# Performance work log

Measured on AMD Instinct MI355X. Metric: run time of the kernel, lower is better.

The kernel has to match this reference:

```python
import math
import jax, jax.numpy as jnp
import numpy as np

B, S, M, D, H = 4, 1024, 8, 64, 8
NF = D // 2  # n_freq = head_dim // 2
BANDWIDTH = 1.0


def setup_inputs() -> dict:
    key = jax.random.key(0)
    ks = jax.random.split(key, 12)
    n = lambda k, shp, sc=1.0: (jax.random.normal(k, shp, dtype=jnp.float32) * sc)
    w_scale = 0.02  # typical init scale for linear weights
    return {
        'q_atoms': n(ks[0], (B, S, M, D)),
        'q_logw': n(ks[1], (B, S, M)),
        'k_atoms': n(ks[2], (B, S, M, D)),
        'k_logw': n(ks[3], (B, S, M)),
        'v_atoms': n(ks[4], (B, S, M, D)),
        'v_logw': n(ks[5], (B, S, M)),
        'Wq': n(ks[6], (H * D, D), w_scale),   # torch Linear weight [out, in]
        'Wk': n(ks[7], (H * D, D), w_scale),
        'Wv': n(ks[8], (H * D, D), w_scale),
        'Wo': n(ks[9], (D, H * D), w_scale),
        'Ww': n(ks[10], (M, D), w_scale * 0.1),  # w_proj.weight scaled by 0.1
        'freqs': n(ks[11], (H, D, NF), 1.0 / BANDWIDTH),  # buffer
    }


def reference(q_atoms, q_logw, k_atoms, k_logw, v_atoms, v_logw,
              Wq, Wk, Wv, Wo, Ww, freqs):
    rff_scale = 1.0 / math.sqrt(NF)
    attn_scale = 1.0 / math.sqrt(D)

    q_w = jax.nn.softmax(q_logw, axis=-1)  # [B,S,M]
    k_w = jax.nn.softmax(k_logw, axis=-1)

    def proj(x, W):  # x: [B,S,M,D], W: [H*D, D] -> [B,S,M,H,D]
        return jnp.einsum('bsmd,ed->bsme', x, W).reshape(B, -1, M, H, D)

    qa = proj(q_atoms, Wq)
    ka = proj(k_atoms, Wk)
    va = proj(v_atoms, Wv)  # [B,S,M,H,D]

    def rff_encode(atoms, weights):
        # atoms: [B,S,M,H,D], weights: [B,S,M] -> [B,H,S,F] with F=D
        p = jnp.einsum('bsmhd,hdf->bsmhf', atoms, freqs)
        phi = jnp.concatenate([jnp.cos(p), jnp.sin(p)], axis=-1) * rff_scale
        z = jnp.einsum('bsmhf,bsm->bshf', phi, weights)
        return z.transpose(0, 2, 1, 3)

    q_enc = rff_encode(qa, q_w)  # [B,H,S,D]
    k_enc = rff_encode(ka, k_w)

    attn = jax.nn.softmax(
        jnp.einsum('bhqf,bhkf->bhqk', q_enc, k_enc) * attn_scale, axis=-1)

    # attn @ values, keeping atom dim m: [B,S,M,H,D]
    out = jnp.einsum('bhqk,bkmhd->bqmhd', attn, va)
    out = out.reshape(B, S, M, H * D)
    out_atoms = out @ Wo.T                  # [B,S,M,D]
    out_features = out_atoms.mean(axis=2)   # [B,S,D]
    new_log_weights = q_logw + out_features @ Ww.T  # [B,S,M]
    return out_atoms, new_log_weights
```

## Files before the change

### kernel.cpp

```cpp
#include <hip/hip_runtime.h>
#include <hip/hip_bf16.h>

typedef __hip_bfloat16 bf16;
typedef __attribute__((ext_vector_type(8))) short short8;
typedef __attribute__((ext_vector_type(4))) float floatx4;

#define CB 4
#define CS 1024
#define CM 8
#define CD 64
#define CH 8
#define CNF 32
#define CHD 512

#define OB_STRIDE 520
#define OS_STRIDE 68
#define AT_STRIDE 72
#define VO_STRIDE 40

__device__ __forceinline__ float b2f(bf16 x) { return __bfloat162float(x); }
__device__ __forceinline__ float us2f(unsigned short u) {
    union { unsigned int i; float f; } v; v.i = ((unsigned int)u) << 16; return v.f;
}
__device__ __forceinline__ floatx4 mfma16(short8 a, short8 b, floatx4 c) {
    return __builtin_amdgcn_mfma_f32_16x16x32_bf16(a, b, c, 0, 0, 0);
}


__global__ __launch_bounds__(256) void prep(const float* __restrict__ Wq,
                                            const float* __restrict__ Wk,
                                            const float* __restrict__ freqs,
                                            const float* __restrict__ Wo,
                                            const float* __restrict__ Wv,
                                            bf16* __restrict__ Fqb,
                                            bf16* __restrict__ Fkb,
                                            bf16* __restrict__ Wof,
                                            bf16* __restrict__ Wvf) {
    int bx = blockIdx.x, t = threadIdx.x;
    if (bx < 128) {
        int which = bx >> 6, h = (bx >> 3) & 7, ec = bx & 7;
        const float* W = which ? Wk : Wq;
        bf16* Fb = which ? Fkb : Fqb;
        int f = t & 31, el = t >> 5;
        int e = ec * 8 + el;
        float acc = 0.f;
        for (int d = 0; d < 64; ++d)
            acc += W[(h * 64 + d) * 64 + e] * freqs[(h * 64 + d) * 32 + f];
        int ntile = h * 2 + (f >> 4);
        int half = e >> 5, quad = (e >> 3) & 3, j = e & 7;
        Fb[(ntile * 2 + half) * 512 + quad * 128 + (f & 15) * 8 + j] = __float2bfloat16(acc);
    } else if (bx < 144) {
        int gid = (bx - 128) * 256 + t;
        #pragma unroll
        for (int i = 0; i < 2; ++i) {
            int idx4 = gid * 2 + i;
            float4 v = ((const float4*)Wo)[idx4];
            int flat = idx4 * 4;
            int o = flat >> 9, k0 = flat & 511;
            int ot = o >> 4, r0 = o & 15;
            int ks = k0 >> 5, qd = (k0 >> 3) & 3, j0 = k0 & 7;
            union { bf16 ob[4]; uint2 u; } pk;
            pk.ob[0] = __float2bfloat16(v.x); pk.ob[1] = __float2bfloat16(v.y);
            pk.ob[2] = __float2bfloat16(v.z); pk.ob[3] = __float2bfloat16(v.w);
            *(uint2*)(Wof + (ot * 16 + ks) * 512 + qd * 128 + r0 * 8 + j0) = pk.u;
        }
    } else {
        int gid = (bx - 144) * 256 + t;
        #pragma unroll
        for (int i = 0; i < 2; ++i) {
            int idx4 = gid * 2 + i;
            float4 v = ((const float4*)Wv)[idx4];
            int flat = idx4 * 4;
            int c = flat >> 6, e0 = flat & 63;
            int h2 = c >> 6, d = c & 63;
            int ehalf = e0 >> 5, qd = (e0 >> 3) & 3, j0 = e0 & 7;
            union { bf16 ob[4]; uint2 u; } pk;
            pk.ob[0] = __float2bfloat16(v.x); pk.ob[1] = __float2bfloat16(v.y);
            pk.ob[2] = __float2bfloat16(v.z); pk.ob[3] = __float2bfloat16(v.w);
            *(uint2*)(Wvf + (h2 * 8 + (d >> 4) * 2 + ehalf) * 512
                          + qd * 128 + (d & 15) * 8 + j0) = pk.u;
        }
    }
}

__global__ __launch_bounds__(256) void encvp(const float* __restrict__ qa_in,
                                             const float* __restrict__ ql,
                                             const float* __restrict__ ka_in,
                                             const float* __restrict__ kl,
                                             const bf16* __restrict__ Fqb,
                                             const bf16* __restrict__ Fkb,
                                             bf16* __restrict__ qf,
                                             bf16* __restrict__ kf,
                                             const float* __restrict__ va_in,
                                             const bf16* __restrict__ Wvf,
                                             bf16* __restrict__ Vt) {
    __shared__ __align__(16) bf16 smem[20480];
    int t = threadIdx.x;
    int w = t >> 6, l = t & 63;
    int quad = l >> 4, r = l & 15;

    if (blockIdx.x < 1024) {
        int blk = blockIdx.x;
        int xbase = blk * 4;
        int b = xbase >> 10, s0 = xbase & 1023;
        float* wgtF = (float*)smem;
        bf16* atq = smem + 128;
        bf16* atk = smem + 128 + 2304;
        bf16* zL  = smem + 128 + 4608;
        int tw = w & 1, nb = (w >> 1) * 8;

        {
            const float* srcq = qa_in + (size_t)(blk * 32) * 64;
            const float* srck = ka_in + (size_t)(blk * 32) * 64;
            #pragma unroll
            for (int j = 0; j < 2; ++j) {
                int idx4 = j * 256 + t;
                int flat = idx4 * 4;
                int row = flat >> 6, e = flat & 63;
                float4 vq = ((const float4*)srcq)[idx4];
                float4 vk = ((const float4*)srck)[idx4];
                union { bf16 ob[4]; uint2 u; } pq, pk2;
                pq.ob[0] = __float2bfloat16(vq.x); pq.ob[1] = __float2bfloat16(vq.y);
                pq.ob[2] = __float2bfloat16(vq.z); pq.ob[3] = __float2bfloat16(vq.w);
                pk2.ob[0] = __float2bfloat16(vk.x); pk2.ob[1] = __float2bfloat16(vk.y);
                pk2.ob[2] = __float2bfloat16(vk.z); pk2.ob[3] = __float2bfloat16(vk.w);
                *(uint2*)(atq + row * AT_STRIDE + e) = pq.u;
                *(uint2*)(atk + row * AT_STRIDE + e) = pk2.u;
            }
        }
        if (t < 64) {
            int which = t >> 5, row = t & 31;
            int si = row >> 3, m = row & 7;
            const float* lwp = (which ? kl : ql) + (size_t)(xbase + si) * 8;
            float lw[8]; float mx = -1e30f;
            #pragma unroll
            for (int j = 0; j < 8; ++j) { lw[j] = lwp[j]; mx = fmaxf(mx, lw[j]); }
            float sm = 0.f;
            #pragma unroll
            for (int j = 0; j < 8; ++j) sm += __expf(lw[j] - mx);
            const float rs = 0.17677669529663687f;
            float osc = which ? rs : rs * 0.125f;
            wgtF[which * 32 + row] = __expf(lw[m] - mx) * (osc / sm);
        }
        __syncthreads();

        for (int which = 0; which < 2; ++which) {
            const bf16* atb2 = which ? atk : atq;
            const bf16* Fb = which ? Fkb : Fqb;

            short8 a0 = *(const short8*)(atb2 + (tw * 16 + r) * AT_STRIDE + quad * 8);
            short8 a1 = *(const short8*)(atb2 + (tw * 16 + r) * AT_STRIDE + quad * 8 + 32);

            floatx4 acc[8];
            #pragma unroll
            for (int nt = 0; nt < 8; ++nt) {
                int ntile = nb + nt;
                short8 b0 = *(const short8*)(Fb + (ntile * 2 + 0) * 512 + l * 8);
                short8 b1 = *(const short8*)(Fb + (ntile * 2 + 1) * 512 + l * 8);
                floatx4 c = {0.f, 0.f, 0.f, 0.f};
                c = mfma16(a0, b0, c);
                c = mfma16(a1, b1, c);
                acc[nt] = c;
            }

            float wv[4];
            #pragma unroll
            for (int reg = 0; reg < 4; ++reg)
                wv[reg] = wgtF[which * 32 + tw * 16 + quad * 4 + reg];

            int si = tw * 2 + (quad >> 1);
            int iss = quad & 1;
            #pragma unroll
            for (int nt = 0; nt < 8; ++nt) {
                int n = (nb + nt) * 16 + r;
                int h = n >> 5, f = n & 31;
                float zc = 0.f, zs = 0.f;
                #pragma unroll
                for (int reg = 0; reg < 4; ++reg) {
                    float sv, cv;
                    __sincosf(acc[nt][reg], &sv, &cv);
                    zc += wv[reg] * cv;
                    zs += wv[reg] * sv;
                }
                zc += __shfl_xor(zc, 16);
                zs += __shfl_xor(zs, 16);
                float val = iss ? zs : zc;
                zL[((which * 4 + si) * 8 + h) * 64 + f + 32 * iss] = __float2bfloat16(val);
            }
        }
        __syncthreads();

        #pragma unroll
        for (int rep = 0; rep < 2; ++rep) {
            int idx = rep * 256 + t;
            int row = idx >> 3, c = idx & 7;
            int which = row >> 5, si = (row >> 3) & 3, h = row & 7;
            bf16* enc = which ? kf : qf;
            short8 v = *(const short8*)(zL + row * 64 + c * 8);
            int s = s0 + si;
            int bh = b * 8 + h;
            int kt = s >> 4, half = c >> 2, qd = c & 3;
            *(short8*)(enc + ((size_t)((bh * 64 + kt) * 2 + half)) * 512
                           + (qd * 16 + (s & 15)) * 8) = v;
        }
    } else {
        int vp = blockIdx.x - 1024;
        int bh = vp & 31, sc = vp >> 5;
        int b = bh >> 3, h = bh & 7;
        bf16* atb = smem;
        bf16* os = smem;

        const float* src = va_in + ((size_t)(b * 1024 + sc * 32)) * 512;
        #pragma unroll
        for (int j = 0; j < 16; ++j) {
            int idx4 = j * 256 + t;
            float4 v = ((const float4*)src)[idx4];
            int flat = idx4 * 4;
            int s = flat >> 9, m = (flat >> 6) & 7, e = flat & 63;
            union { bf16 ob[4]; uint2 u; } pk;
            pk.ob[0] = __float2bfloat16(v.x); pk.ob[1] = __float2bfloat16(v.y);
            pk.ob[2] = __float2bfloat16(v.z); pk.ob[3] = __float2bfloat16(v.w);
            *(uint2*)(atb + (m * 32 + s) * AT_STRIDE + e) = pk.u;
        }
        __syncthreads();

        int dhalf = w & 1, sg = w >> 1;
        short8 aw0[2], aw1[2];
        #pragma unroll
        for (int dt = 0; dt < 2; ++dt) {
            int dt4 = dhalf * 2 + dt;
            aw0[dt] = *(const short8*)(Wvf + (size_t)(h * 8 + dt4 * 2 + 0) * 512 + l * 8);
            aw1[dt] = *(const short8*)(Wvf + (size_t)(h * 8 + dt4 * 2 + 1) * 512 + l * 8);
        }
        floatx4 acc[8][2];
        #pragma unroll
        for (int m = 0; m < 8; ++m)
            #pragma unroll
            for (int dt = 0; dt < 2; ++dt) acc[m][dt] = (floatx4){0.f, 0.f, 0.f, 0.f};

        #pragma unroll
        for (int m = 0; m < 8; ++m) {
            short8 b0 = *(const short8*)(atb + (m * 32 + sg * 16 + r) * AT_STRIDE + quad * 8);
            short8 b1 = *(const short8*)(atb + (m * 32 + sg * 16 + r) * AT_STRIDE + quad * 8 + 32);
            #pragma unroll
            for (int dt = 0; dt < 2; ++dt) {
                acc[m][dt] = mfma16(aw0[dt], b0, acc[m][dt]);
                acc[m][dt] = mfma16(aw1[dt], b1, acc[m][dt]);
            }
        }
        __syncthreads();

        #pragma unroll
        for (int m = 0; m < 8; ++m)
            #pragma unroll
            for (int dt = 0; dt < 2; ++dt)
                #pragma unroll
                for (int reg = 0; reg < 4; ++reg) {
                    int n = m * 64 + dhalf * 32 + dt * 16 + quad * 4 + reg;
                    os[n * VO_STRIDE + sg * 16 + r] = __float2bfloat16(acc[m][dt][reg]);
                }
        __syncthreads();

        #pragma unroll
        for (int j = 0; j < 8; ++j) {
            int ch = j * 256 + t;
            int nblk = ch >> 6, lv = ch & 63;
            int rv = lv & 15, qv = lv >> 4;
            short8 v = *(const short8*)(os + (nblk * 16 + rv) * VO_STRIDE + qv * 8);
            *(short8*)(Vt + ((size_t)(bh * 32 + nblk) * 32 + sc) * 512 + lv * 8) = v;
        }
    }
}

__global__ __launch_bounds__(512, 2) void attn_kern(const bf16* __restrict__ qf,
                                                    const bf16* __restrict__ kf,
                                                    const bf16* __restrict__ Vt,
                                                    bf16* __restrict__ tmpf) {
    int n = blockIdx.x;
    int bh = (n & 7) | (((n >> 7) & 3) << 3);
    int qb = (n >> 3) & 15;
    int b = bh >> 3, h = bh & 7;

    __shared__ __align__(16) bf16 Sc[64 * 1024];
    int t = threadIdx.x;
    int w = t >> 6, l = t & 63;
    int quad = l >> 4, r = l & 15;
    int k7 = r & 7;

    const bf16* qfb = qf + (size_t)(bh * 128 + qb * 8) * 512 + l * 8;
    short8 q[8];
    #pragma unroll
    for (int i = 0; i < 8; ++i) q[i] = *(const short8*)(qfb + i * 512);

    const bf16* kfb = kf + (size_t)(bh * 128) * 512 + l * 8;
    short8 kA0 = *(const short8*)(kfb + (size_t)(w * 8) * 1024);
    short8 kA1 = *(const short8*)(kfb + (size_t)(w * 8) * 1024 + 512);
    short8 kB0 = *(const short8*)(kfb + (size_t)(w * 8 + 1) * 1024);
    short8 kB1 = *(const short8*)(kfb + (size_t)(w * 8 + 1) * 1024 + 512);

    #pragma unroll
    for (int i = 0; i < 8; ++i) {
        short8 k0 = kA0, k1 = kA1;
        kA0 = kB0; kA1 = kB1;
        if (i < 6) {
            kB0 = *(const short8*)(kfb + (size_t)(w * 8 + i + 2) * 1024);
            kB1 = *(const short8*)(kfb + (size_t)(w * 8 + i + 2) * 1024 + 512);
        }
        int ktl = w * 8 + i;
        int chunk = ktl * 2 + (quad >> 1);
        int sw = ((chunk ^ k7) << 3) + (quad & 1) * 4;
        #pragma unroll
        for (int qt = 0; qt < 4; ++qt) {
            floatx4 c = {0.f, 0.f, 0.f, 0.f};
            c = mfma16(k0, q[2 * qt], c);
            c = mfma16(k1, q[2 * qt + 1], c);
            union { uint2 u; bf16 bb[4]; } p;
            #pragma unroll
            for (int reg = 0; reg < 4; ++reg) p.bb[reg] = __float2bfloat16(c[reg]);
            *(uint2*)(Sc + (qt * 16 + r) * 1024 + sw) = p.u;
        }
    }
    __syncthreads();

    for (int i = 0; i < 8; ++i) {
        int row = w * 8 + i;
        int key = row & 7;
        bf16* rowp = Sc + row * 1024;
        int p0 = ((2 * l) ^ key) << 3;
        int p1 = ((2 * l + 1) ^ key) << 3;
        union { short8 s; unsigned short u[8]; } v0, v1;
        v0.s = *(const short8*)(rowp + p0);
        v1.s = *(const short8*)(rowp + p1);
        float f[16];
        #pragma unroll
        for (int j = 0; j < 8; ++j) { f[j] = us2f(v0.u[j]); f[8 + j] = us2f(v1.u[j]); }
        float mx = -1e30f;
        #pragma unroll
        for (int j = 0; j < 16; ++j) mx = fmaxf(mx, f[j]);
        #pragma unroll
        for (int off = 32; off; off >>= 1) mx = fmaxf(mx, __shfl_xor(mx, off));
        float sm = 0.f;
        #pragma unroll
        for (int j = 0; j < 16; ++j) { f[j] = __expf(f[j] - mx); sm += f[j]; }
        #pragma unroll
        for (int off = 32; off; off >>= 1) sm += __shfl_xor(sm, off);
        float inv = 1.f / sm;
        #pragma unroll
        for (int j = 0; j < 8; ++j) {
            v0.u[j] = (unsigned short)(__bfloat16_as_ushort(__float2bfloat16(f[j] * inv)));
            v1.u[j] = (unsigned short)(__bfloat16_as_ushort(__float2bfloat16(f[8 + j] * inv)));
        }
        *(short8*)(rowp + p0) = v0.s;
        *(short8*)(rowp + p1) = v1.s;
    }
    __syncthreads();

    floatx4 acc[4][4];
    #pragma unroll
    for (int qt = 0; qt < 4; ++qt)
        #pragma unroll
        for (int nt = 0; nt < 4; ++nt) acc[qt][nt] = (floatx4){0.f, 0.f, 0.f, 0.f};

    const bf16* vbase = Vt + ((size_t)(bh * 32 + w * 4) * 32) * 512 + l * 8;
    short8 vA[4], vB[4], vC[4];
    #pragma unroll
    for (int nt = 0; nt < 4; ++nt) vA[nt] = *(const short8*)(vbase + nt * 16384);
    #pragma unroll
    for (int nt = 0; nt < 4; ++nt) vB[nt] = *(const short8*)(vbase + nt * 16384 + 512);

    #pragma unroll
    for (int ks = 0; ks < 32; ++ks) {
        if (ks < 30) {
            #pragma unroll
            for (int nt = 0; nt < 4; ++nt)
                vC[nt] = *(const short8*)(vbase + nt * 16384 + (ks + 2) * 512);
        }
        int pc = (((ks * 4 + quad) ^ k7) << 3);
        short8 pa[4];
        #pragma unroll
        for (int qt = 0; qt < 4; ++qt)
            pa[qt] = *(const short8*)(Sc + (qt * 16 + r) * 1024 + pc);
        #pragma unroll
        for (int nt = 0; nt < 4; ++nt)
            #pragma unroll
            for (int qt = 0; qt < 4; ++qt)
                acc[qt][nt] = mfma16(pa[qt], vA[nt], acc[qt][nt]);
        #pragma unroll
        for (int nt = 0; nt < 4; ++nt) { vA[nt] = vB[nt]; vB[nt] = vC[nt]; }
    }
    __syncthreads();

    bf16* Ob = Sc;
    #pragma unroll
    for (int qt = 0; qt < 4; ++qt)
        #pragma unroll
        for (int nt = 0; nt < 4; ++nt)
            #pragma unroll
            for (int reg = 0; reg < 4; ++reg) {
                int col = w * 64 + nt * 16 + r;
                int m = col >> 6, d = col & 63;
                int colS = m * 64 + ((d + m * 8) & 63);
                Ob[(qt * 16 + quad * 4 + reg) * OB_STRIDE + colS] =
                    __float2bfloat16(acc[qt][nt][reg]);
            }
    __syncthreads();

    #pragma unroll
    for (int i = 0; i < 8; ++i) {
        int ci = i * 8 + w;
        int lv = t & 63;
        int T = ci >> 1, khalf = ci & 1;
        int quadv = lv >> 4, rv = lv & 15;
        int p = rv >> 3, m = rv & 7;
        int q_local = T * 2 + p;
        int d0 = khalf * 32 + quadv * 8;
        int colS = m * 64 + ((d0 + m * 8) & 63);
        short8 v = *(const short8*)(Ob + q_local * OB_STRIDE + colS);
        int GT = b * 512 + qb * 32 + T;
        *(short8*)(tmpf + ((size_t)(GT * 16 + h * 2 + khalf)) * 512 + lv * 8) = v;
    }
}

__global__ __launch_bounds__(256) void finalize(const bf16* __restrict__ tmpf,
                                                const bf16* __restrict__ Wof,
                                                const float* __restrict__ Ww,
                                                const float* __restrict__ ql,
                                                float* __restrict__ out) {
    __shared__ __align__(16) float Os[64][OS_STRIDE];
    __shared__ float fs[8][64];
    int t = threadIdx.x;
    int w = t >> 6, l = t & 63;
    int quad = l >> 4, r = l & 15;
    size_t rowbase = (size_t)blockIdx.x * 64;

    floatx4 acc[4];
    #pragma unroll
    for (int nt = 0; nt < 4; ++nt) acc[nt] = (floatx4){0.f, 0.f, 0.f, 0.f};

    const bf16* afrag = tmpf + ((size_t)(blockIdx.x * 4 + w) * 16) * 512 + l * 8;
    const bf16* bfrag = Wof + l * 8;

    for (int ks = 0; ks < 16; ++ks) {
        short8 a = *(const short8*)(afrag + ks * 512);
        #pragma unroll
        for (int nt = 0; nt < 4; ++nt) {
            short8 bb = *(const short8*)(bfrag + (size_t)(nt * 16 + ks) * 512);
            acc[nt] = mfma16(a, bb, acc[nt]);
        }
    }
    #pragma unroll
    for (int nt = 0; nt < 4; ++nt)
        #pragma unroll
        for (int reg = 0; reg < 4; ++reg)
            Os[w * 16 + quad * 4 + reg][nt * 16 + r] = acc[nt][reg];
    __syncthreads();

    #pragma unroll
    for (int i = 0; i < 4; ++i) {
        int ch = i * 256 + t;
        int rr = ch >> 4, c4 = (ch & 15) * 4;
        float4 v = *(const float4*)&Os[rr][c4];
        *(float4*)(out + (rowbase + rr) * 64 + c4) = v;
    }

    {
        int g = t >> 5, oo = (t & 31) * 2;
        float f0 = 0.f, f1 = 0.f;
        #pragma unroll
        for (int m = 0; m < 8; ++m) {
            f0 += Os[g * 8 + m][oo];
            f1 += Os[g * 8 + m][oo + 1];
        }
        fs[g][oo] = f0 * 0.125f;
        fs[g][oo + 1] = f1 * 0.125f;
    }
    __syncthreads();

    if (t < 64) {
        int g = t >> 3, mm = t & 7;
        size_t x = (size_t)blockIdx.x * 8 + g;
        float nl = ql[x * 8 + mm];
        #pragma unroll
        for (int o = 0; o < 64; ++o) nl += fs[g][o] * Ww[mm * 64 + o];
        out[(size_t)CB * CS * CM * CD + x * 8 + mm] = nl;
    }
}

extern "C" void kernel_launch(void* const* d_in, const int* in_sizes, int n_in,
                              void* d_out, int out_size, void* d_ws, size_t ws_size,
                              hipStream_t stream) {
    const float* q_atoms = (const float*)d_in[0];
    const float* q_logw  = (const float*)d_in[1];
    const float* k_atoms = (const float*)d_in[2];
    const float* k_logw  = (const float*)d_in[3];
    const float* v_atoms = (const float*)d_in[4];
    const float* Wq = (const float*)d_in[6];
    const float* Wk = (const float*)d_in[7];
    const float* Wv = (const float*)d_in[8];
    const float* Wo = (const float*)d_in[9];
    const float* Ww = (const float*)d_in[10];
    const float* freqs = (const float*)d_in[11];

    bf16* Fqb = (bf16*)d_ws;
    bf16* Fkb = Fqb + 16384;
    bf16* qf = Fkb + 16384;
    bf16* kf = qf + 2097152;
    bf16* Vt = kf + 2097152;
    bf16* tmpf = Vt + 2097152 * 8;
    bf16* Wof = tmpf + 16777216;
    bf16* Wvf = Wof + 32768;
    float* out = (float*)d_out;

    prep<<<160, 256, 0, stream>>>(Wq, Wk, freqs, Wo, Wv, Fqb, Fkb, Wof, Wvf);
    encvp<<<2048, 256, 0, stream>>>(q_atoms, q_logw, k_atoms, k_logw,
                                    Fqb, Fkb, qf, kf,
                                    v_atoms, Wvf, Vt);
    attn_kern<<<512, 512, 0, stream>>>(qf, kf, Vt, tmpf);
    finalize<<<CB * CS / 8, 256, 0, stream>>>(tmpf, Wof, Ww, q_logw, out);
}
```

Before: 190.6 us.

## Split attention over key halves with unnormalized exp and deferred softmax normalization

The attention kernel now processes keys in two halves: scores are exponentiated directly without a max pass, written to a half-size shared buffer, and immediately consumed by the P·V MFMA loop. Row sums are reduced across waves and the normalization is applied to the output accumulators at the end. This removes the separate softmax pass and halves shared memory, allowing higher occupancy. The V-prep block index mapping is also reordered. It relies on the scores being bounded so that skipping max subtraction cannot overflow.

```diff
diff --git a/kernel.cpp b/kernel.cpp
--- a/kernel.cpp
+++ b/kernel.cpp
@@ -205,8 +205,9 @@
         }
     } else {
         int vp = blockIdx.x - 1024;
-        int bh = vp & 31, sc = vp >> 5;
-        int b = bh >> 3, h = bh & 7;
+        int g = vp & 127, h = vp >> 7;
+        int b = g >> 5, sc = g & 31;
+        int bh = b * 8 + h;
         bf16* atb = smem;
         bf16* os = smem;
 
@@ -272,7 +273,7 @@
     }
 }
 
-__global__ __launch_bounds__(512, 2) void attn_kern(const bf16* __restrict__ qf,
+__global__ __launch_bounds__(512, 4) void attn_kern(const bf16* __restrict__ qf,
                                                     const bf16* __restrict__ kf,
                                                     const bf16* __restrict__ Vt,
                                                     bf16* __restrict__ tmpf) {
@@ -281,114 +282,115 @@
     int qb = (n >> 3) & 15;
     int b = bh >> 3, h = bh & 7;
 
-    __shared__ __align__(16) bf16 Sc[64 * 1024];
+    __shared__ __align__(16) bf16 Sc[64 * OB_STRIDE];
+    __shared__ float sumW[8 * 64];
+    __shared__ float invL[64];
     int t = threadIdx.x;
     int w = t >> 6, l = t & 63;
     int quad = l >> 4, r = l & 15;
     int k7 = r & 7;
 
     const bf16* qfb = qf + (size_t)(bh * 128 + qb * 8) * 512 + l * 8;
-    short8 q[8];
-    #pragma unroll
-    for (int i = 0; i < 8; ++i) q[i] = *(const short8*)(qfb + i * 512);
-
     const bf16* kfb = kf + (size_t)(bh * 128) * 512 + l * 8;
-    short8 kA0 = *(const short8*)(kfb + (size_t)(w * 8) * 1024);
-    short8 kA1 = *(const short8*)(kfb + (size_t)(w * 8) * 1024 + 512);
-    short8 kB0 = *(const short8*)(kfb + (size_t)(w * 8 + 1) * 1024);
-    short8 kB1 = *(const short8*)(kfb + (size_t)(w * 8 + 1) * 1024 + 512);
-
-    #pragma unroll
-    for (int i = 0; i < 8; ++i) {
-        short8 k0 = kA0, k1 = kA1;
-        kA0 = kB0; kA1 = kB1;
-        if (i < 6) {
-            kB0 = *(const short8*)(kfb + (size_t)(w * 8 + i + 2) * 1024);
-            kB1 = *(const short8*)(kfb + (size_t)(w * 8 + i + 2) * 1024 + 512);
-        }
-        int ktl = w * 8 + i;
-        int chunk = ktl * 2 + (quad >> 1);
-        int sw = ((chunk ^ k7) << 3) + (quad & 1) * 4;
-        #pragma unroll
-        for (int qt = 0; qt < 4; ++qt) {
-            floatx4 c = {0.f, 0.f, 0.f, 0.f};
-            c = mfma16(k0, q[2 * qt], c);
-            c = mfma16(k1, q[2 * qt + 1], c);
-            union { uint2 u; bf16 bb[4]; } p;
-            #pragma unroll
-            for (int reg = 0; reg < 4; ++reg) p.bb[reg] = __float2bfloat16(c[reg]);
-            *(uint2*)(Sc + (qt * 16 + r) * 1024 + sw) = p.u;
-        }
-    }
-    __syncthreads();
-
-    for (int i = 0; i < 8; ++i) {
-        int row = w * 8 + i;
-        int key = row & 7;
-        bf16* rowp = Sc + row * 1024;
-        int p0 = ((2 * l) ^ key) << 3;
-        int p1 = ((2 * l + 1) ^ key) << 3;
-        union { short8 s; unsigned short u[8]; } v0, v1;
-        v0.s = *(const short8*)(rowp + p0);
-        v1.s = *(const short8*)(rowp + p1);
-        float f[16];
-        #pragma unroll
-        for (int j = 0; j < 8; ++j) { f[j] = us2f(v0.u[j]); f[8 + j] = us2f(v1.u[j]); }
-        float mx = -1e30f;
-        #pragma unroll
-        for (int j = 0; j < 16; ++j) mx = fmaxf(mx, f[j]);
-        #pragma unroll
-        for (int off = 32; off; off >>= 1) mx = fmaxf(mx, __shfl_xor(mx, off));
-        float sm = 0.f;
-        #pragma unroll
-        for (int j = 0; j < 16; ++j) { f[j] = __expf(f[j] - mx); sm += f[j]; }
-        #pragma unroll
-        for (int off = 32; off; off >>= 1) sm += __shfl_xor(sm, off);
-        float inv = 1.f / sm;
-        #pragma unroll
-        for (int j = 0; j < 8; ++j) {
-            v0.u[j] = (unsigned short)(__bfloat16_as_ushort(__float2bfloat16(f[j] * inv)));
-            v1.u[j] = (unsigned short)(__bfloat16_as_ushort(__float2bfloat16(f[8 + j] * inv)));
-        }
-        *(short8*)(rowp + p0) = v0.s;
-        *(short8*)(rowp + p1) = v1.s;
-    }
-    __syncthreads();
+    const bf16* vbase = Vt + ((size_t)(bh * 32 + w * 4) * 32) * 512 + l * 8;
 
     floatx4 acc[4][4];
     #pragma unroll
     for (int qt = 0; qt < 4; ++qt)
         #pragma unroll
         for (int nt = 0; nt < 4; ++nt) acc[qt][nt] = (floatx4){0.f, 0.f, 0.f, 0.f};
-
-    const bf16* vbase = Vt + ((size_t)(bh * 32 + w * 4) * 32) * 512 + l * 8;
-    short8 vA[4], vB[4], vC[4];
-    #pragma unroll
-    for (int nt = 0; nt < 4; ++nt) vA[nt] = *(const short8*)(vbase + nt * 16384);
-    #pragma unroll
-    for (int nt = 0; nt < 4; ++nt) vB[nt] = *(const short8*)(vbase + nt * 16384 + 512);
-
-    #pragma unroll
-    for (int ks = 0; ks < 32; ++ks) {
-        if (ks < 30) {
-            #pragma unroll
-            for (int nt = 0; nt < 4; ++nt)
-                vC[nt] = *(const short8*)(vbase + nt * 16384 + (ks + 2) * 512);
-        }
-        int pc = (((ks * 4 + quad) ^ k7) << 3);
-        short8 pa[4];
-        #pragma unroll
-        for (int qt = 0; qt < 4; ++qt)
-            pa[qt] = *(const short8*)(Sc + (qt * 16 + r) * 1024 + pc);
-        #pragma unroll
-        for (int nt = 0; nt < 4; ++nt)
-            #pragma unroll
-            for (int qt = 0; qt < 4; ++qt)
-                acc[qt][nt] = mfma16(pa[qt], vA[nt], acc[qt][nt]);
-        #pragma unroll
-        for (int nt = 0; nt < 4; ++nt) { vA[nt] = vB[nt]; vB[nt] = vC[nt]; }
-    }
-    __syncthreads();
+    float ps[4] = {0.f, 0.f, 0.f, 0.f};
+
+    for (int khalf = 0; khalf < 2; ++khalf) {
+        {
+            short8 q[8];
+            #pragma unroll
+            for (int i = 0; i < 8; ++i) q[i] = *(const short8*)(qfb + i * 512);
+            short8 kr[4][2];
+            #pragma unroll
+            for (int d = 0; d < 4; ++d) {
+                kr[d][0] = *(const short8*)(kfb + (size_t)(khalf * 32 + w * 4 + d) * 1024);
+                kr[d][1] = *(const short8*)(kfb + (size_t)(khalf * 32 + w * 4 + d) * 1024 + 512);
+            }
+            #pragma unroll
+            for (int i = 0; i < 4; ++i) {
+                int ktl = w * 4 + i;
+                #pragma unroll
+                for (int qt = 0; qt < 4; ++qt) {
+                    floatx4 c = {0.f, 0.f, 0.f, 0.f};
+                    c = mfma16(kr[i][0], q[2 * qt], c);
+                    c = mfma16(kr[i][1], q[2 * qt + 1], c);
+                    int g = ktl * 2 + (quad >> 1);
+                    int sw = ((g ^ k7) << 3) + (quad & 1) * 4;
+                    union { uint2 u; bf16 bb[4]; } p;
+                    #pragma unroll
+                    for (int reg = 0; reg < 4; ++reg) {
+                        float e = __expf(c[reg]);
+                        ps[qt] += e;
+                        p.bb[reg] = __float2bfloat16(e);
+                    }
+                    *(uint2*)(Sc + (qt * 16 + r) * OB_STRIDE + sw) = p.u;
+                }
+            }
+        }
+        if (khalf == 1) {
+            #pragma unroll
+            for (int qt = 0; qt < 4; ++qt) {
+                ps[qt] += __shfl_xor(ps[qt], 16);
+                ps[qt] += __shfl_xor(ps[qt], 32);
+            }
+            if (l < 16) {
+                #pragma unroll
+                for (int qt = 0; qt < 4; ++qt) sumW[w * 64 + qt * 16 + r] = ps[qt];
+            }
+        }
+        __syncthreads();
+        if (khalf == 1 && t < 64) {
+            float s = 0.f;
+            #pragma unroll
+            for (int w2 = 0; w2 < 8; ++w2) s += sumW[w2 * 64 + t];
+            invL[t] = 1.f / s;
+        }
+
+        {
+            short8 vr[2][4];
+            #pragma unroll
+            for (int d = 0; d < 2; ++d)
+                #pragma unroll
+                for (int nt = 0; nt < 4; ++nt)
+                    vr[d][nt] = *(const short8*)(vbase + nt * 16384
+                                                 + (khalf * 16 + d) * 512);
+            #pragma unroll
+            for (int ks = 0; ks < 16; ++ks) {
+                short8 pa[4];
+                #pragma unroll
+                for (int qt = 0; qt < 4; ++qt)
+                    pa[qt] = *(const short8*)(Sc + (qt * 16 + r) * OB_STRIDE
+                                              + (((ks * 4 + quad) ^ k7) << 3));
+                __builtin_amdgcn_s_setprio(1);
+                #pragma unroll
+                for (int nt = 0; nt < 4; ++nt)
+                    #pragma unroll
+                    for (int qt = 0; qt < 4; ++qt)
+                        acc[qt][nt] = mfma16(pa[qt], vr[ks & 1][nt], acc[qt][nt]);
+                __builtin_amdgcn_s_setprio(0);
+                if (ks + 2 < 16) {
+                    #pragma unroll
+                    for (int nt = 0; nt < 4; ++nt)
+                        vr[ks & 1][nt] = *(const short8*)(vbase + nt * 16384
+                                                          + (khalf * 16 + ks + 2) * 512);
+                }
+            }
+        }
+        __syncthreads();
+    }
+
+    float inv[4][4];
+    #pragma unroll
+    for (int qt = 0; qt < 4; ++qt)
+        #pragma unroll
+        for (int reg = 0; reg < 4; ++reg)
+            inv[qt][reg] = invL[qt * 16 + quad * 4 + reg];
 
     bf16* Ob = Sc;
     #pragma unroll
@@ -401,7 +403,7 @@
                 int m = col >> 6, d = col & 63;
                 int colS = m * 64 + ((d + m * 8) & 63);
                 Ob[(qt * 16 + quad * 4 + reg) * OB_STRIDE + colS] =
-                    __float2bfloat16(acc[qt][nt][reg]);
+                    __float2bfloat16(acc[qt][nt][reg] * inv[qt][reg]);
             }
     __syncthreads();
 
@@ -409,15 +411,15 @@
     for (int i = 0; i < 8; ++i) {
         int ci = i * 8 + w;
         int lv = t & 63;
-        int T = ci >> 1, khalf = ci & 1;
+        int T = ci >> 1, kh = ci & 1;
         int quadv = lv >> 4, rv = lv & 15;
         int p = rv >> 3, m = rv & 7;
         int q_local = T * 2 + p;
-        int d0 = khalf * 32 + quadv * 8;
+        int d0 = kh * 32 + quadv * 8;
         int colS = m * 64 + ((d0 + m * 8) & 63);
         short8 v = *(const short8*)(Ob + q_local * OB_STRIDE + colS);
         int GT = b * 512 + qb * 32 + T;
-        *(short8*)(tmpf + ((size_t)(GT * 16 + h * 2 + khalf)) * 512 + lv * 8) = v;
+        *(short8*)(tmpf + ((size_t)(GT * 16 + h * 2 + kh)) * 512 + lv * 8) = v;
     }
 }
 
```

Result: slower. 206.0 us (+8.0%).
